# Optimization experiments

Measured on AMD Instinct MI355X. Metric: run time of the kernel, lower is better.

The kernel has to match this reference:

```python
import jax, jax.numpy as jnp
import numpy as np

B, S, D, H = 8, 1024, 512, 8
HD = D // H
NEG = -1000000000.0
LN_EPS = 1e-5


def setup_inputs() -> dict:
    key = jax.random.key(0)
    ks = jax.random.split(key, 16)
    sc = 0.02
    inp = {
        "query": jax.random.normal(ks[0], (B, S, D), jnp.float32),
        "inputs": jax.random.normal(ks[1], (B, S, D), jnp.float32),
        "ren_mat": jax.random.uniform(ks[2], (B, S, S), jnp.float32) * 5.0,
        "timestamp": jax.random.normal(ks[3], (B, S, S), jnp.float32),
        # causal mask: True where attention is disallowed (strictly upper triangular)
        "mask": jnp.triu(jnp.ones((1, S, S), jnp.bool_), k=1),
        "Wq": jax.random.normal(ks[4], (D, D), jnp.float32) * sc,
        "bq": jnp.zeros((D,), jnp.float32),
        "Wk": jax.random.normal(ks[5], (D, D), jnp.float32) * sc,
        "bk": jnp.zeros((D,), jnp.float32),
        "Wv": jax.random.normal(ks[6], (D, D), jnp.float32) * sc,
        "bv": jnp.zeros((D,), jnp.float32),
        "Wo": jax.random.normal(ks[7], (D, D), jnp.float32) * sc,
        "bo": jnp.zeros((D,), jnp.float32),
        "W1": jax.random.normal(ks[8], (D, D), jnp.float32) * sc,
        "b1": jnp.zeros((D,), jnp.float32),
        "ln_g": jnp.ones((D,), jnp.float32),
        "ln_b": jnp.zeros((D,), jnp.float32),
        "l1": jax.random.uniform(ks[9], (1,), jnp.float32),
    }
    return inp


def reference(query, inputs, ren_mat, timestamp, mask,
              Wq, bq, Wk, bk, Wv, bv, Wo, bo, W1, b1, ln_g, ln_b, l1):
    # QKV projections (qk_same=False path; q,k,v all computed from `inputs`)
    def proj(x, W, b):
        return (x @ W.T + b).reshape(B, S, H, HD).transpose(0, 2, 1, 3)  # (B,H,S,HD)

    q = proj(inputs, Wq, bq)
    k = proj(inputs, Wk, bk)
    v = proj(inputs, Wv, bv)

    m = mask[:, None]  # (1,1,S,S), broadcasts over batch & heads

    scores = jnp.einsum("bhqd,bhkd->bhqk", q, k) / jnp.sqrt(jnp.float32(HD))
    scores = jnp.where(m, NEG, scores)
    prob_attn = jax.nn.softmax(scores, axis=-1)

    # memory blend: log10(ren+1) and exp(-|t|), each masked, summed, softmaxed
    ren_feat = jnp.where(m, NEG, jnp.log10(ren_mat + 1.0)[:, None])      # (B,H,S,S)
    time_stamp = jnp.where(m, NEG, jnp.exp(-jnp.abs(timestamp))[:, None])
    mem_attn = jax.nn.softmax(ren_feat + time_stamp, axis=-1)

    l = l1  # (1,) learned blend coefficient
    prob_attn = (1.0 - l) * prob_attn + l * mem_attn

    out = jnp.einsum("bhqk,bhkd->bhqd", prob_attn, v)
    out = out.transpose(0, 2, 1, 3).reshape(B, S, D)
    out = out @ Wo.T + bo

    # residual FFN + layernorm (dropout disabled / eval mode)
    out = out + (out @ W1.T + b1)
    mu = jnp.mean(out, axis=-1, keepdims=True)
    var = jnp.var(out, axis=-1, keepdims=True)
    out = (out - mu) / jnp.sqrt(var + LN_EPS) * ln_g + ln_b
    return out
```

## Files before the change

kernel.cpp:

```cpp
#include <hip/hip_runtime.h>
#include <math.h>

constexpr int kB = 8, kS = 1024, kD = 512, kH = 8, kHD = 64;
constexpr int kM = kB * kS;

typedef __attribute__((ext_vector_type(8))) short s8v;
typedef __attribute__((ext_vector_type(4))) float f4v;
typedef __attribute__((ext_vector_type(4))) unsigned short u4v;

__device__ __forceinline__ unsigned short f2bf(float f) {
    union { float f; unsigned int u; } c; c.f = f;
    unsigned int u = c.u + 0x7FFFu + ((c.u >> 16) & 1u);
    return (unsigned short)(u >> 16);
}

__device__ __forceinline__ void gl2lds(const unsigned short* g, unsigned short* l) {
    __builtin_amdgcn_global_load_lds(
        (const __attribute__((address_space(1))) unsigned int*)g,
        (__attribute__((address_space(3))) unsigned int*)l, 16, 0, 0);
}

__global__ __launch_bounds__(256) void prep_kernel(
    const float* __restrict__ X, const float* __restrict__ Wq,
    const float* __restrict__ Wk, const float* __restrict__ Wv,
    const float* __restrict__ Wo, const float* __restrict__ W1,
    const float* __restrict__ ren, const float* __restrict__ ts,
    const float* __restrict__ bo_g,
    unsigned short* __restrict__ Xbf, unsigned short* __restrict__ Wqkv,
    unsigned short* __restrict__ WoT, unsigned short* __restrict__ W1bf,
    unsigned short* __restrict__ mem)
{
    __shared__ float red[4];
    const int t = threadIdx.x;
    if (blockIdx.x < 5120) {
        const int idx = blockIdx.x * 256 + t;
        const float* src; unsigned short* dst; int off; bool isw1 = false;
        if (idx < 1048576)      { src = X;  dst = Xbf;           off = idx; }
        else if (idx < 1114112) { src = Wq; dst = Wqkv;          off = idx - 1048576; }
        else if (idx < 1179648) { src = Wk; dst = Wqkv + 262144; off = idx - 1114112; }
        else if (idx < 1245184) { src = Wv; dst = Wqkv + 524288; off = idx - 1179648; }
        else                    { src = W1; dst = W1bf;          off = idx - 1245184; isw1 = true; }
        float4 v = ((const float4*)src)[off];
        if (isw1) {
            const int e0 = off * 4;
            const int row = e0 >> 9, col0 = e0 & 511;
            if (row >= col0 && row < col0 + 4) ((float*)&v)[row - col0] += 1.0f;
        }
        u4v p;
        p[0] = f2bf(v.x); p[1] = f2bf(v.y); p[2] = f2bf(v.z); p[3] = f2bf(v.w);
        ((u4v*)dst)[off] = p;
        return;
    }
    if (blockIdx.x >= 13312) {
        const int bi2 = blockIdx.x - 13312;
        if (bi2 < 64) {
            __shared__ float T[64][65];
            const int tr = bi2 >> 3, tc = bi2 & 7;
            const int rr0 = t >> 4, cc0 = (t & 15) * 4;
#pragma unroll
            for (int i2 = 0; i2 < 4; ++i2) {
                const int r = i2 * 16 + rr0;
                const float4 v = *(const float4*)&Wo[(size_t)(tr * 64 + r) * 512 + tc * 64 + cc0];
                T[r][cc0] = v.x; T[r][cc0 + 1] = v.y; T[r][cc0 + 2] = v.z; T[r][cc0 + 3] = v.w;
            }
            __syncthreads();
#pragma unroll
            for (int i2 = 0; i2 < 4; ++i2) {
                const int r2 = i2 * 16 + rr0;
                u4v p;
                p[0] = f2bf(T[cc0][r2]);     p[1] = f2bf(T[cc0 + 1][r2]);
                p[2] = f2bf(T[cc0 + 2][r2]); p[3] = f2bf(T[cc0 + 3][r2]);
                *(u4v*)&WoT[(size_t)(tc * 64 + r2) * 512 + tr * 64 + cc0] = p;
            }
        } else {
            WoT[262144 + t]       = f2bf(bo_g[t]);
            WoT[262144 + 256 + t] = f2bf(bo_g[t + 256]);
        }
        return;
    }
    const int bi = blockIdx.x - 5120;
    const int i = bi & (kS - 1);
    const float* renr = ren + (size_t)bi * kS;
    const float* tsr  = ts  + (size_t)bi * kS;
    unsigned short* memr = mem + (size_t)bi * kS;
    const int j0 = t * 4;
    const float4 r4 = *(const float4*)(renr + j0);
    const float4 t4 = *(const float4*)(tsr + j0);
    float rv[4] = {r4.x, r4.y, r4.z, r4.w};
    float tv[4] = {t4.x, t4.y, t4.z, t4.w};
    float p4[4];
    float lsum = 0.0f;
#pragma unroll
    for (int e = 0; e < 4; ++e) {
        const int j = j0 + e;
        float p = 0.0f;
        if (j <= i) {
            const float val = 0.30102999566f * __log2f(rv[e] + 1.0f) + __expf(-fabsf(tv[e]));
            p = __expf(val);
        }
        p4[e] = p;
        lsum += p;
    }
#pragma unroll
    for (int d = 1; d < 64; d <<= 1) lsum += __shfl_xor(lsum, d);
    if ((t & 63) == 0) red[t >> 6] = lsum;
    __syncthreads();
    const float Z = red[0] + red[1] + red[2] + red[3];
    const float inv = 1.0f / Z;
    u4v pk;
#pragma unroll
    for (int e = 0; e < 4; ++e) pk[e] = f2bf(p4[e] * inv);
    *(u4v*)(memr + j0) = pk;
}

template <int NT>
__device__ __forceinline__ void mfma_core2(
    const unsigned short* __restrict__ A, const unsigned short* __restrict__ B,
    int M0, int N0, unsigned short* As, unsigned short* Bs, f4v (&acc)[4][NT])
{
    const int t = threadIdx.x, w = t >> 6, lane = t & 63;
    const int l16 = lane & 15, quad = lane >> 4;
    const int wm = (w & 1) * 64, wn = (w >> 1) * (NT * 16);
    constexpr int NB = NT / 2;
    constexpr int ABUF = 128 * 32;
    constexpr int BBUF = NT * 32 * 32;

    const unsigned short* gA[2]; unsigned short* lA[2];
#pragma unroll
    for (int i = 0; i < 2; ++i) {
        const int r0 = w * 32 + i * 16;
        const int r = r0 + (lane >> 2);
        const int c = (lane & 3) ^ ((r >> 1) & 3);
        gA[i] = A + (size_t)(M0 + r) * 512 + c * 8;
        lA[i] = As + r0 * 32;
    }
    const unsigned short* gB[NB]; unsigned short* lB[NB];
#pragma unroll
    for (int i = 0; i < NB; ++i) {
        const int r0 = w * (16 * NB) + i * 16;
        const int r = r0 + (lane >> 2);
        const int c = (lane & 3) ^ ((r >> 1) & 3);
        gB[i] = B + (size_t)(N0 + r) * 512 + c * 8;
        lB[i] = Bs + r0 * 32;
    }

    const f4v zero = {0.0f, 0.0f, 0.0f, 0.0f};
#pragma unroll
    for (int mt = 0; mt < 4; ++mt)
#pragma unroll
        for (int nt = 0; nt < NT; ++nt) acc[mt][nt] = zero;

    gl2lds(gA[0], lA[0]);
    gl2lds(gA[1], lA[1]);
#pragma unroll
    for (int i = 0; i < NB; ++i) gl2lds(gB[i], lB[i]);

#pragma unroll 1
    for (int k0 = 0; k0 < 512; k0 += 32) {
        const int cur = (k0 >> 5) & 1;
        __syncthreads();
        if (k0 + 32 < 512) {
            const int nb = cur ^ 1;
            gl2lds(gA[0] + k0 + 32, lA[0] + nb * ABUF);
            gl2lds(gA[1] + k0 + 32, lA[1] + nb * ABUF);
#pragma unroll
            for (int i = 0; i < NB; ++i) gl2lds(gB[i] + k0 + 32, lB[i] + nb * BBUF);
        }
        s8v af[4], bf_[NT];
#pragma unroll
        for (int mt = 0; mt < 4; ++mt) {
            const int r = wm + mt * 16 + l16;
            const int p = r * 4 + (quad ^ ((r >> 1) & 3));
            af[mt] = *(const s8v*)&As[cur * ABUF + p * 8];
        }
#pragma unroll
        for (int nt = 0; nt < NT; ++nt) {
            const int r = wn + nt * 16 + l16;
            const int p = r * 4 + (quad ^ ((r >> 1) & 3));
            bf_[nt] = *(const s8v*)&Bs[cur * BBUF + p * 8];
        }
#pragma unroll
        for (int mt = 0; mt < 4; ++mt)
#pragma unroll
            for (int nt = 0; nt < NT; ++nt)
                acc[mt][nt] = __builtin_amdgcn_mfma_f32_16x16x32_bf16(
                    af[mt], bf_[nt], acc[mt][nt], 0, 0, 0);
    }
}

__global__ __launch_bounds__(256) void qkv_mfma_kernel(
    const unsigned short* __restrict__ Xbf, const unsigned short* __restrict__ Wqkv,
    const float* __restrict__ bq, const float* __restrict__ bk, const float* __restrict__ bv,
    const unsigned short* __restrict__ W1bf, const unsigned short* __restrict__ WoT,
    const float* __restrict__ b1,
    unsigned short* __restrict__ qbf, unsigned short* __restrict__ kbf,
    unsigned short* __restrict__ vTbf,
    unsigned short* __restrict__ Wcomb, float* __restrict__ bcomb)
{
    __shared__ __align__(16) unsigned short As[2 * 128 * 32];
    __shared__ __align__(16) unsigned short Bs[2 * 128 * 32];
    const int y = blockIdx.y;
    const int t = threadIdx.x, w = t >> 6, lane = t & 63;
    const int l16 = lane & 15, quad = lane >> 4;

    if (y == 12) {
        if (blockIdx.x >= 36) return;
        f4v acc[4][2];
        const int M0 = (blockIdx.x / 9) * 128, N0 = (blockIdx.x % 9) * 64;
        mfma_core2<2>(W1bf, WoT, M0, N0, As, Bs, acc);
        const int wm = (w & 1) * 64, wn = (w >> 1) * 32;
#pragma unroll
        for (int nt = 0; nt < 2; ++nt) {
            const int qq = N0 + wn + nt * 16 + l16;
#pragma unroll
            for (int mt = 0; mt < 4; ++mt)
#pragma unroll
                for (int rr = 0; rr < 4; ++rr) {
                    const int m = M0 + wm + mt * 16 + quad * 4 + rr;
                    if (qq < 512)       Wcomb[(size_t)m * 512 + qq] = f2bf(acc[mt][nt][rr]);
                    else if (qq == 512) bcomb[m] = acc[mt][nt][rr] + b1[m];
                }
        }
        return;
    }

    f4v acc[4][4];
    const int wm = (w & 1) * 64, wn = (w >> 1) * 64;
    if (y < 8) {
        const int M0 = blockIdx.x * 128, N0 = y * 128;
        mfma_core2<4>(Xbf, Wqkv, M0, N0, As, Bs, acc);
        const int z = N0 >> 9;
        const float* bias = (z == 0) ? bq : bk;
        unsigned short* out = (z == 0) ? qbf : kbf;
#pragma unroll
        for (int nt = 0; nt < 4; ++nt) {
            const int n512 = (N0 + wn + nt * 16 + l16) & 511;
            const int h = n512 >> 6, hd = n512 & 63;
            const float bv_ = bias[n512];
#pragma unroll
            for (int mt = 0; mt < 4; ++mt) {
#pragma unroll
                for (int rr = 0; rr < 4; ++rr) {
                    const int m = M0 + wm + mt * 16 + quad * 4 + rr;
                    const int b = m >> 10, s = m & (kS - 1);
                    out[(((size_t)b * kH + h) * kS + s) * kHD + hd] =
                        f2bf(acc[mt][nt][rr] + bv_);
                }
            }
        }
    } else {
        const int M0 = (y - 8) * 128, N0 = blockIdx.x * 128;
        mfma_core2<4>(Wqkv + (size_t)1024 * 512, Xbf, M0, N0, As, Bs, acc);
#pragma unroll
        for (int mt = 0; mt < 4; ++mt) {
#pragma unroll
            for (int rr = 0; rr < 4; ++rr) {
                const int vcol = M0 + wm + mt * 16 + quad * 4 + rr;
                const int h = vcol >> 6, hd = vcol & 63;
                const float bv_ = bv[vcol];
#pragma unroll
                for (int nt = 0; nt < 4; ++nt) {
                    const int sg = N0 + wn + nt * 16 + l16;
                    const int b = sg >> 10, s = sg & (kS - 1);
                    vTbf[(((size_t)b * kH + h) * kHD + hd) * kS + s] =
                        f2bf(acc[mt][nt][rr] + bv_);
                }
            }
        }
    }
}

__global__ __launch_bounds__(256) void gemm_final_kernel(
    const unsigned short* __restrict__ Abf, const unsigned short* __restrict__ Wcomb,
    const float* __restrict__ bcomb, float* __restrict__ out)
{
    __shared__ __align__(16) unsigned short As[2 * 128 * 32];
    __shared__ __align__(16) unsigned short Bs[2 * 64 * 32];
    f4v acc[4][2];
    const int M0 = blockIdx.x * 128, N0 = blockIdx.y * 64;
    mfma_core2<2>(Abf, Wcomb, M0, N0, As, Bs, acc);
    const int t = threadIdx.x, w = t >> 6, lane = t & 63;
    const int l16 = lane & 15, quad = lane >> 4;
    const int wm = (w & 1) * 64, wn = (w >> 1) * 32;
#pragma unroll
    for (int nt = 0; nt < 2; ++nt) {
        const int n = N0 + wn + nt * 16 + l16;
        const float bv_ = bcomb[n];
#pragma unroll
        for (int mt = 0; mt < 4; ++mt)
#pragma unroll
            for (int rr = 0; rr < 4; ++rr) {
                const int m = M0 + wm + mt * 16 + quad * 4 + rr;
                out[(size_t)m * kD + n] = acc[mt][nt][rr] + bv_;
            }
    }
}

#define KFRAG(tile, r, c) (*(const s8v*)&(tile)[(size_t)(r) * 64 + ((((c) ^ ((r) & 7))) << 3)])
#define VFRAG(tile, r, c) (*(const s8v*)&(tile)[(size_t)(r) * 128 + ((((c) ^ ((r) & 15))) << 3)])

__global__ __launch_bounds__(256, 2) void flash_attn_kernel(
    const unsigned short* __restrict__ q, const unsigned short* __restrict__ k,
    const unsigned short* __restrict__ vT, const unsigned short* __restrict__ mem,
    const float* __restrict__ l1, unsigned short* __restrict__ aout)
{
    const int bh = blockIdx.x;
    const int qt = 15 - blockIdx.y;
    const int b = bh >> 3, h = bh & 7;
    const int t = threadIdx.x;
    const int w = t >> 6, lane = t & 63;
    const int quad = lane >> 4, l16 = lane & 15;
    const float lam = l1[0];

    __shared__ __align__(16) unsigned short KV[2][2][64 * 128];
    __shared__ __align__(16) unsigned short P_lds[4][16 * 128];

    const int qbase = qt * 64;
    const unsigned short* qrow = q + ((size_t)bh * kS + qbase + w * 16 + l16) * kHD;
    const s8v qa0 = *(const s8v*)(qrow + quad * 8);
    const s8v qa1 = *(const s8v*)(qrow + 32 + quad * 8);
    const unsigned short* mbase = mem + ((size_t)b * kS + qbase + w * 16 + l16) * kS;

    const unsigned short* kb = k + (size_t)bh * kS * kHD;
    const unsigned short* vb = vT + (size_t)bh * kHD * kS;

    const int nkt = (qt >> 1) + 1;

    const unsigned short* gsrc[8];
    int gstep[8];
    unsigned short* ldst[8];
#pragma unroll
    for (int u = 0; u < 8; ++u) {
        const int seg = w * 8 + u;
        if (seg < 16) {
            const int s = seg;
            const int rloc = s * 8 + (lane >> 3);
            const int chunk = (lane & 7) ^ ((lane >> 3) & 7);
            gsrc[u] = kb + (size_t)rloc * kHD + chunk * 8;
            gstep[u] = 128 * kHD;
            ldst[u] = &KV[0][0][s * 512];
        } else {
            const int s = seg - 16;
            const int d = s * 4 + (lane >> 4);
            const int chunk = (lane & 15) ^ ((lane >> 4) & 3) ^ ((s & 3) << 2);
            gsrc[u] = vb + (size_t)d * kS + chunk * 8;
            gstep[u] = 128;
            ldst[u] = &KV[0][1][s * 512];
        }
    }

#pragma unroll
    for (int u = 0; u < 8; ++u) gl2lds(gsrc[u], ldst[u]);

    const f4v zero = {0.0f, 0.0f, 0.0f, 0.0f};
    f4v Oa[4], Om[4];
    float lr[4];
#pragma unroll
    for (int nt = 0; nt < 4; ++nt) { Oa[nt] = zero; Om[nt] = zero; lr[nt] = 0.0f; }

    for (int kt = 0; kt < nkt; ++kt) {
        __syncthreads();
        const int cur = kt & 1;
        if (kt + 1 < nkt) {
            const int boff = ((kt + 1) & 1) * 16384;
#pragma unroll
            for (int u = 0; u < 8; ++u)
                gl2lds(gsrc[u] + (size_t)(kt + 1) * gstep[u], ldst[u] + boff);
        }
        s8v ma[4];
#pragma unroll
        for (int ks = 0; ks < 4; ++ks)
            ma[ks] = *(const s8v*)(mbase + kt * 128 + ks * 32 + quad * 8);

        const unsigned short* Kc = &KV[cur][0][0];
        const unsigned short* Vc = &KV[cur][1][0];
        const bool last = (kt == nkt - 1);

#pragma unroll
        for (int ct = 0; ct < 8; ++ct) {
            const int r = ct * 16 + l16;
            const s8v kb0 = KFRAG(Kc, r, quad);
            const s8v kb1 = KFRAG(Kc, r, 4 + quad);
            f4v acc = zero;
            acc = __builtin_amdgcn_mfma_f32_16x16x32_bf16(qa0, kb0, acc, 0, 0, 0);
            acc = __builtin_amdgcn_mfma_f32_16x16x32_bf16(qa1, kb1, acc, 0, 0, 0);
#pragma unroll
            for (int rr = 0; rr < 4; ++rr) {
                float p = __expf(acc[rr] * 0.125f);
                if (last && (kt * 128 + r) > (qbase + w * 16 + quad * 4 + rr)) p = 0.0f;
                lr[rr] += p;
                const int pr = quad * 4 + rr;
                const int ck = ct * 2 + (l16 >> 3);
                P_lds[w][pr * 128 + (((ck ^ pr) & 15) << 3) + (l16 & 7)] = f2bf(p);
            }
        }
        s8v pa[4];
#pragma unroll
        for (int ks = 0; ks < 4; ++ks)
            pa[ks] = *(const s8v*)&P_lds[w][l16 * 128 + ((((ks * 4 + quad) ^ l16) & 15) << 3)];
#pragma unroll
        for (int nt = 0; nt < 4; ++nt) {
#pragma unroll
            for (int ks = 0; ks < 4; ++ks) {
                const s8v vfk = VFRAG(Vc, nt * 16 + l16, ks * 4 + quad);
                Oa[nt] = __builtin_amdgcn_mfma_f32_16x16x32_bf16(pa[ks], vfk, Oa[nt], 0, 0, 0);
                Om[nt] = __builtin_amdgcn_mfma_f32_16x16x32_bf16(ma[ks], vfk, Om[nt], 0, 0, 0);
            }
        }
    }

    float inv4[4];
#pragma unroll
    for (int rr = 0; rr < 4; ++rr) {
        float Z = lr[rr];
        Z += __shfl_xor(Z, 1);
        Z += __shfl_xor(Z, 2);
        Z += __shfl_xor(Z, 4);
        Z += __shfl_xor(Z, 8);
        inv4[rr] = (1.0f - lam) / Z;
    }
    const int r0 = qbase + w * 16;
#pragma unroll
    for (int nt = 0; nt < 4; ++nt)
#pragma unroll
        for (int rr = 0; rr < 4; ++rr) {
            const int i = r0 + quad * 4 + rr;
            const int d = h * kHD + nt * 16 + l16;
            aout[((size_t)b * kS + i) * kD + d] =
                f2bf(Oa[nt][rr] * inv4[rr] + lam * Om[nt][rr]);
        }
}

__global__ __launch_bounds__(256) void ln_kernel(
    const float* __restrict__ x, const float* __restrict__ g,
    const float* __restrict__ bb, float* __restrict__ out)
{
    const int row = blockIdx.x;
    const int t = threadIdx.x;
    const float* xr = x + (size_t)row * kD;
    float a = xr[t], c = xr[t + 256];
    __shared__ float red[256];
    float s1 = a + c, s2 = a * a + c * c;
    red[t] = s1;
    __syncthreads();
    for (int s = 128; s > 0; s >>= 1) {
        if (t < s) red[t] += red[t + s];
        __syncthreads();
    }
    const float sum = red[0];
    __syncthreads();
    red[t] = s2;
    __syncthreads();
    for (int s = 128; s > 0; s >>= 1) {
        if (t < s) red[t] += red[t + s];
        __syncthreads();
    }
    const float sq = red[0];
    float mu = sum * (1.0f / kD);
    float var = sq * (1.0f / kD) - mu * mu;
    float inv = rsqrtf(var + 1e-5f);
    out[(size_t)row * kD + t]       = (a - mu) * inv * g[t] + bb[t];
    out[(size_t)row * kD + t + 256] = (c - mu) * inv * g[t + 256] + bb[t + 256];
}

extern "C" void kernel_launch(void* const* d_in, const int* in_sizes, int n_in,
                              void* d_out, int out_size, void* d_ws, size_t ws_size,
                              hipStream_t stream) {
    const float* X   = (const float*)d_in[1];
    const float* ren = (const float*)d_in[2];
    const float* ts  = (const float*)d_in[3];
    const float* Wq = (const float*)d_in[5];  const float* bq = (const float*)d_in[6];
    const float* Wk = (const float*)d_in[7];  const float* bk = (const float*)d_in[8];
    const float* Wv = (const float*)d_in[9];  const float* bv = (const float*)d_in[10];
    const float* Wo = (const float*)d_in[11]; const float* bo = (const float*)d_in[12];
    const float* W1 = (const float*)d_in[13]; const float* b1 = (const float*)d_in[14];
    const float* lng = (const float*)d_in[15]; const float* lnb = (const float*)d_in[16];
    const float* l1 = (const float*)d_in[17];
    float* out = (float*)d_out;

    char* wsb = (char*)d_ws;
    unsigned short* Xbf    = (unsigned short*)(wsb);
    unsigned short* Wqkvbf = (unsigned short*)(wsb + (8u  << 20));
    unsigned short* WoTbf  = (unsigned short*)(wsb + (10u << 20));
    unsigned short* W1bf   = (unsigned short*)(wsb + (11u << 20));
    unsigned short* qbf    = (unsigned short*)(wsb + (12u << 20));
    unsigned short* kbf    = (unsigned short*)(wsb + (20u << 20));
    unsigned short* vTbf   = (unsigned short*)(wsb + (28u << 20));
    unsigned short* membf  = (unsigned short*)(wsb + (36u << 20));
    unsigned short* aoutbf = (unsigned short*)(wsb + (52u << 20));
    unsigned short* Wcombf = (unsigned short*)(wsb + (60u << 20));
    float*          bcombf = (float*)        (wsb + (61u << 20));

    prep_kernel<<<dim3(13377), 256, 0, stream>>>(
        X, Wq, Wk, Wv, Wo, W1, ren, ts, bo, Xbf, Wqkvbf, WoTbf, W1bf, membf);
    qkv_mfma_kernel<<<dim3(kM / 128, 13), 256, 0, stream>>>(
        Xbf, Wqkvbf, bq, bk, bv, W1bf, WoTbf, b1, qbf, kbf, vTbf, Wcombf, bcombf);
    flash_attn_kernel<<<dim3(64, 16), 256, 0, stream>>>(
        qbf, kbf, vTbf, membf, l1, aoutbf);
    gemm_final_kernel<<<dim3(kM / 128, kD / 64), 256, 0, stream>>>(
        aoutbf, Wcombf, bcombf, out);
    ln_kernel<<<dim3(kM), 256, 0, stream>>>(out, lng, lnb, out);
}
```

Baseline: 249.1 us.

## Fuse final GEMM with layernorm, pair causal query tiles, skip masked mem loads

Replaces the separate output GEMM and layernorm kernels with one kernel where each block computes a full 32x512 row tile and reduces mean and variance in registers and shared memory. This removes the fp32 round trip of the pre-norm output. The attention kernel now pairs a high and a low causal query tile in each block so every block does the same amount of work and the K/V tiles are loaded once for both. The prep kernel also skips reading ren and timestamp for fully masked column chunks. In exchange, the fused GEMM launches fewer, larger blocks, and the attention kernel holds two sets of accumulators, which raises register pressure.

```diff
diff --git a/kernel.cpp b/kernel.cpp
--- a/kernel.cpp
+++ b/kernel.cpp
@@ -84,22 +84,24 @@
     const float* tsr  = ts  + (size_t)bi * kS;
     unsigned short* memr = mem + (size_t)bi * kS;
     const int j0 = t * 4;
-    const float4 r4 = *(const float4*)(renr + j0);
-    const float4 t4 = *(const float4*)(tsr + j0);
-    float rv[4] = {r4.x, r4.y, r4.z, r4.w};
-    float tv[4] = {t4.x, t4.y, t4.z, t4.w};
-    float p4[4];
+    float p4[4] = {0.0f, 0.0f, 0.0f, 0.0f};
     float lsum = 0.0f;
-#pragma unroll
-    for (int e = 0; e < 4; ++e) {
-        const int j = j0 + e;
-        float p = 0.0f;
-        if (j <= i) {
-            const float val = 0.30102999566f * __log2f(rv[e] + 1.0f) + __expf(-fabsf(tv[e]));
-            p = __expf(val);
-        }
-        p4[e] = p;
-        lsum += p;
+    if (j0 <= i) {
+        const float4 r4 = *(const float4*)(renr + j0);
+        const float4 t4 = *(const float4*)(tsr + j0);
+        float rv[4] = {r4.x, r4.y, r4.z, r4.w};
+        float tv[4] = {t4.x, t4.y, t4.z, t4.w};
+#pragma unroll
+        for (int e = 0; e < 4; ++e) {
+            const int j = j0 + e;
+            float p = 0.0f;
+            if (j <= i) {
+                const float val = 0.30102999566f * __log2f(rv[e] + 1.0f) + __expf(-fabsf(tv[e]));
+                p = __expf(val);
+            }
+            p4[e] = p;
+            lsum += p;
+        }
     }
 #pragma unroll
     for (int d = 1; d < 64; d <<= 1) lsum += __shfl_xor(lsum, d);
@@ -270,30 +272,135 @@
     }
 }
 
-__global__ __launch_bounds__(256) void gemm_final_kernel(
+__global__ __launch_bounds__(512, 2) void gemm_ln_kernel(
     const unsigned short* __restrict__ Abf, const unsigned short* __restrict__ Wcomb,
-    const float* __restrict__ bcomb, float* __restrict__ out)
+    const float* __restrict__ bcomb, const float* __restrict__ g,
+    const float* __restrict__ bb, float* __restrict__ out)
 {
-    __shared__ __align__(16) unsigned short As[2 * 128 * 32];
-    __shared__ __align__(16) unsigned short Bs[2 * 64 * 32];
-    f4v acc[4][2];
-    const int M0 = blockIdx.x * 128, N0 = blockIdx.y * 64;
-    mfma_core2<2>(Abf, Wcomb, M0, N0, As, Bs, acc);
+    __shared__ __align__(16) unsigned short As[2 * 32 * 32];
+    __shared__ __align__(16) unsigned short Bs[2 * 512 * 32];
+    constexpr int ABUF = 32 * 32, BBUF = 512 * 32;
     const int t = threadIdx.x, w = t >> 6, lane = t & 63;
     const int l16 = lane & 15, quad = lane >> 4;
-    const int wm = (w & 1) * 64, wn = (w >> 1) * 32;
-#pragma unroll
-    for (int nt = 0; nt < 2; ++nt) {
-        const int n = N0 + wn + nt * 16 + l16;
-        const float bv_ = bcomb[n];
-#pragma unroll
-        for (int mt = 0; mt < 4; ++mt)
-#pragma unroll
-            for (int rr = 0; rr < 4; ++rr) {
-                const int m = M0 + wm + mt * 16 + quad * 4 + rr;
-                out[(size_t)m * kD + n] = acc[mt][nt][rr] + bv_;
-            }
-    }
+    const int M0 = blockIdx.x * 32;
+
+    const unsigned short* gB[4]; unsigned short* lB[4];
+#pragma unroll
+    for (int i = 0; i < 4; ++i) {
+        const int r0 = w * 64 + i * 16;
+        const int r = r0 + (lane >> 2);
+        const int c = (lane & 3) ^ ((r >> 1) & 3);
+        gB[i] = Wcomb + (size_t)r * 512 + c * 8;
+        lB[i] = Bs + r0 * 32;
+    }
+    const unsigned short* gA = nullptr; unsigned short* lA = nullptr;
+    if (w < 2) {
+        const int r0 = w * 16;
+        const int r = r0 + (lane >> 2);
+        const int c = (lane & 3) ^ ((r >> 1) & 3);
+        gA = Abf + (size_t)(M0 + r) * 512 + c * 8;
+        lA = As + r0 * 32;
+    }
+
+    const f4v zero = {0.0f, 0.0f, 0.0f, 0.0f};
+    f4v acc[2][4];
+#pragma unroll
+    for (int mt = 0; mt < 2; ++mt)
+#pragma unroll
+        for (int nt = 0; nt < 4; ++nt) acc[mt][nt] = zero;
+
+#pragma unroll
+    for (int i = 0; i < 4; ++i) gl2lds(gB[i], lB[i]);
+    if (w < 2) gl2lds(gA, lA);
+
+#pragma unroll 1
+    for (int k0 = 0; k0 < 512; k0 += 32) {
+        const int cur = (k0 >> 5) & 1;
+        __syncthreads();
+        if (k0 + 32 < 512) {
+            const int nb = cur ^ 1;
+#pragma unroll
+            for (int i = 0; i < 4; ++i) gl2lds(gB[i] + k0 + 32, lB[i] + nb * BBUF);
+            if (w < 2) gl2lds(gA + k0 + 32, lA + nb * ABUF);
+        }
+        s8v af[2], bf_[4];
+#pragma unroll
+        for (int mt = 0; mt < 2; ++mt) {
+            const int r = mt * 16 + l16;
+            const int p = r * 4 + (quad ^ ((r >> 1) & 3));
+            af[mt] = *(const s8v*)&As[cur * ABUF + p * 8];
+        }
+#pragma unroll
+        for (int nt = 0; nt < 4; ++nt) {
+            const int r = w * 64 + nt * 16 + l16;
+            const int p = r * 4 + (quad ^ ((r >> 1) & 3));
+            bf_[nt] = *(const s8v*)&Bs[cur * BBUF + p * 8];
+        }
+#pragma unroll
+        for (int mt = 0; mt < 2; ++mt)
+#pragma unroll
+            for (int nt = 0; nt < 4; ++nt)
+                acc[mt][nt] = __builtin_amdgcn_mfma_f32_16x16x32_bf16(
+                    af[mt], bf_[nt], acc[mt][nt], 0, 0, 0);
+    }
+
+    float bias[4], gg[4], bbv[4];
+#pragma unroll
+    for (int nt = 0; nt < 4; ++nt) {
+        const int n = w * 64 + nt * 16 + l16;
+        bias[nt] = bcomb[n]; gg[nt] = g[n]; bbv[nt] = bb[n];
+    }
+#pragma unroll
+    for (int mt = 0; mt < 2; ++mt)
+#pragma unroll
+        for (int nt = 0; nt < 4; ++nt)
+#pragma unroll
+            for (int rr = 0; rr < 4; ++rr) acc[mt][nt][rr] += bias[nt];
+
+    float2* red = (float2*)Bs;
+    float2* stats = (float2*)As;
+#pragma unroll
+    for (int mt = 0; mt < 2; ++mt)
+#pragma unroll
+        for (int rr = 0; rr < 4; ++rr) {
+            float s = 0.0f, qq = 0.0f;
+#pragma unroll
+            for (int nt = 0; nt < 4; ++nt) {
+                const float v = acc[mt][nt][rr];
+                s += v; qq += v * v;
+            }
+            s += __shfl_xor(s, 1); qq += __shfl_xor(qq, 1);
+            s += __shfl_xor(s, 2); qq += __shfl_xor(qq, 2);
+            s += __shfl_xor(s, 4); qq += __shfl_xor(qq, 4);
+            s += __shfl_xor(s, 8); qq += __shfl_xor(qq, 8);
+            if (l16 == 0) red[w * 32 + mt * 16 + quad * 4 + rr] = make_float2(s, qq);
+        }
+    __syncthreads();
+    if (t < 32) {
+        float s = 0.0f, qq = 0.0f;
+#pragma unroll
+        for (int wv = 0; wv < 8; ++wv) {
+            const float2 f2 = red[wv * 32 + t];
+            s += f2.x; qq += f2.y;
+        }
+        const float mu = s * (1.0f / kD);
+        const float var = qq * (1.0f / kD) - mu * mu;
+        stats[t] = make_float2(mu, rsqrtf(var + 1e-5f));
+    }
+    __syncthreads();
+#pragma unroll
+    for (int mt = 0; mt < 2; ++mt)
+#pragma unroll
+        for (int rr = 0; rr < 4; ++rr) {
+            const int row = mt * 16 + quad * 4 + rr;
+            const float2 st = stats[row];
+#pragma unroll
+            for (int nt = 0; nt < 4; ++nt) {
+                const int n = w * 64 + nt * 16 + l16;
+                out[(size_t)(M0 + row) * kD + n] =
+                    (acc[mt][nt][rr] - st.x) * st.y * gg[nt] + bbv[nt];
+            }
+        }
 }
 
 #define KFRAG(tile, r, c) (*(const s8v*)&(tile)[(size_t)(r) * 64 + ((((c) ^ ((r) & 7))) << 3)])
@@ -304,9 +411,10 @@
     const unsigned short* __restrict__ vT, const unsigned short* __restrict__ mem,
     const float* __restrict__ l1, unsigned short* __restrict__ aout)
 {
-    const int bh = blockIdx.x;
-    const int qt = 15 - blockIdx.y;
-    const int b = bh >> 3, h = bh & 7;
+    const int qp = blockIdx.x;
+    const int hi = 15 - qp, lo = qp;
+    const int h = blockIdx.y, b = blockIdx.z;
+    const int bh = b * kH + h;
     const int t = threadIdx.x;
     const int w = t >> 6, lane = t & 63;
     const int quad = lane >> 4, l16 = lane & 15;
@@ -315,16 +423,22 @@
     __shared__ __align__(16) unsigned short KV[2][2][64 * 128];
     __shared__ __align__(16) unsigned short P_lds[4][16 * 128];
 
-    const int qbase = qt * 64;
-    const unsigned short* qrow = q + ((size_t)bh * kS + qbase + w * 16 + l16) * kHD;
-    const s8v qa0 = *(const s8v*)(qrow + quad * 8);
-    const s8v qa1 = *(const s8v*)(qrow + 32 + quad * 8);
-    const unsigned short* mbase = mem + ((size_t)b * kS + qbase + w * 16 + l16) * kS;
+    const int tbase[2] = {hi * 64, lo * 64};
+    s8v qa[2][2];
+    const unsigned short* mbase[2];
+#pragma unroll
+    for (int ti = 0; ti < 2; ++ti) {
+        const unsigned short* qrow = q + ((size_t)bh * kS + tbase[ti] + w * 16 + l16) * kHD;
+        qa[ti][0] = *(const s8v*)(qrow + quad * 8);
+        qa[ti][1] = *(const s8v*)(qrow + 32 + quad * 8);
+        mbase[ti] = mem + ((size_t)b * kS + tbase[ti] + w * 16 + l16) * kS;
+    }
 
     const unsigned short* kb = k + (size_t)bh * kS * kHD;
     const unsigned short* vb = vT + (size_t)bh * kHD * kS;
 
-    const int nkt = (qt >> 1) + 1;
+    const int nkt   = (hi >> 1) + 1;
+    const int nktlo = (lo >> 1) + 1;
 
     const unsigned short* gsrc[8];
     int gstep[8];
@@ -353,10 +467,14 @@
     for (int u = 0; u < 8; ++u) gl2lds(gsrc[u], ldst[u]);
 
     const f4v zero = {0.0f, 0.0f, 0.0f, 0.0f};
-    f4v Oa[4], Om[4];
-    float lr[4];
-#pragma unroll
-    for (int nt = 0; nt < 4; ++nt) { Oa[nt] = zero; Om[nt] = zero; lr[nt] = 0.0f; }
+    f4v Oa[2][4], Om[2][4];
+    float lr[2][4];
+#pragma unroll
+    for (int ti = 0; ti < 2; ++ti)
+#pragma unroll
+        for (int nt = 0; nt < 4; ++nt) {
+            Oa[ti][nt] = zero; Om[ti][nt] = zero; lr[ti][nt] = 0.0f;
+        }
 
     for (int kt = 0; kt < nkt; ++kt) {
         __syncthreads();
@@ -367,100 +485,107 @@
             for (int u = 0; u < 8; ++u)
                 gl2lds(gsrc[u] + (size_t)(kt + 1) * gstep[u], ldst[u] + boff);
         }
-        s8v ma[4];
+        const bool alo = (kt < nktlo);
+        s8v ma0[4], ma1[4];
 #pragma unroll
         for (int ks = 0; ks < 4; ++ks)
-            ma[ks] = *(const s8v*)(mbase + kt * 128 + ks * 32 + quad * 8);
-
+            ma0[ks] = *(const s8v*)(mbase[0] + kt * 128 + ks * 32 + quad * 8);
+        if (alo) {
+#pragma unroll
+            for (int ks = 0; ks < 4; ++ks)
+                ma1[ks] = *(const s8v*)(mbase[1] + kt * 128 + ks * 32 + quad * 8);
+        }
         const unsigned short* Kc = &KV[cur][0][0];
         const unsigned short* Vc = &KV[cur][1][0];
-        const bool last = (kt == nkt - 1);
-
-#pragma unroll
-        for (int ct = 0; ct < 8; ++ct) {
-            const int r = ct * 16 + l16;
-            const s8v kb0 = KFRAG(Kc, r, quad);
-            const s8v kb1 = KFRAG(Kc, r, 4 + quad);
-            f4v acc = zero;
-            acc = __builtin_amdgcn_mfma_f32_16x16x32_bf16(qa0, kb0, acc, 0, 0, 0);
-            acc = __builtin_amdgcn_mfma_f32_16x16x32_bf16(qa1, kb1, acc, 0, 0, 0);
-#pragma unroll
-            for (int rr = 0; rr < 4; ++rr) {
-                float p = __expf(acc[rr] * 0.125f);
-                if (last && (kt * 128 + r) > (qbase + w * 16 + quad * 4 + rr)) p = 0.0f;
-                lr[rr] += p;
-                const int pr = quad * 4 + rr;
-                const int ck = ct * 2 + (l16 >> 3);
-                P_lds[w][pr * 128 + (((ck ^ pr) & 15) << 3) + (l16 & 7)] = f2bf(p);
-            }
-        }
-        s8v pa[4];
-#pragma unroll
-        for (int ks = 0; ks < 4; ++ks)
-            pa[ks] = *(const s8v*)&P_lds[w][l16 * 128 + ((((ks * 4 + quad) ^ l16) & 15) << 3)];
+
+        s8v pa0[4], pa1[4];
+        {
+            const bool diag = (kt == nkt - 1);
+#pragma unroll
+            for (int ct = 0; ct < 8; ++ct) {
+                const int r = ct * 16 + l16;
+                const s8v kb0 = KFRAG(Kc, r, quad);
+                const s8v kb1 = KFRAG(Kc, r, 4 + quad);
+                f4v acc = zero;
+                acc = __builtin_amdgcn_mfma_f32_16x16x32_bf16(qa[0][0], kb0, acc, 0, 0, 0);
+                acc = __builtin_amdgcn_mfma_f32_16x16x32_bf16(qa[0][1], kb1, acc, 0, 0, 0);
+#pragma unroll
+                for (int rr = 0; rr < 4; ++rr) {
+                    float p = __expf(acc[rr] * 0.125f);
+                    if (diag && (kt * 128 + r) > (tbase[0] + w * 16 + quad * 4 + rr)) p = 0.0f;
+                    lr[0][rr] += p;
+                    const int pr = quad * 4 + rr;
+                    const int ck = ct * 2 + (l16 >> 3);
+                    P_lds[w][pr * 128 + (((ck ^ pr) & 15) << 3) + (l16 & 7)] = f2bf(p);
+                }
+            }
+#pragma unroll
+            for (int ks = 0; ks < 4; ++ks)
+                pa0[ks] = *(const s8v*)&P_lds[w][l16 * 128 + ((((ks * 4 + quad) ^ l16) & 15) << 3)];
+        }
+        if (alo) {
+            const bool diag = (kt == nktlo - 1);
+#pragma unroll
+            for (int ct = 0; ct < 8; ++ct) {
+                const int r = ct * 16 + l16;
+                const s8v kb0 = KFRAG(Kc, r, quad);
+                const s8v kb1 = KFRAG(Kc, r, 4 + quad);
+                f4v acc = zero;
+                acc = __builtin_amdgcn_mfma_f32_16x16x32_bf16(qa[1][0], kb0, acc, 0, 0, 0);
+                acc = __builtin_amdgcn_mfma_f32_16x16x32_bf16(qa[1][1], kb1, acc, 0, 0, 0);
+#pragma unroll
+                for (int rr = 0; rr < 4; ++rr) {
+                    float p = __expf(acc[rr] * 0.125f);
+                    if (diag && (kt * 128 + r) > (tbase[1] + w * 16 + quad * 4 + rr)) p = 0.0f;
+                    lr[1][rr] += p;
+                    const int pr = quad * 4 + rr;
+                    const int ck = ct * 2 + (l16 >> 3);
+                    P_lds[w][pr * 128 + (((ck ^ pr) & 15) << 3) + (l16 & 7)] = f2bf(p);
+                }
+            }
+#pragma unroll
+            for (int ks = 0; ks < 4; ++ks)
+                pa1[ks] = *(const s8v*)&P_lds[w][l16 * 128 + ((((ks * 4 + quad) ^ l16) & 15) << 3)];
+        }
+
 #pragma unroll
         for (int nt = 0; nt < 4; ++nt) {
 #pragma unroll
             for (int ks = 0; ks < 4; ++ks) {
                 const s8v vfk = VFRAG(Vc, nt * 16 + l16, ks * 4 + quad);
-                Oa[nt] = __builtin_amdgcn_mfma_f32_16x16x32_bf16(pa[ks], vfk, Oa[nt], 0, 0, 0);
-                Om[nt] = __builtin_amdgcn_mfma_f32_16x16x32_bf16(ma[ks], vfk, Om[nt], 0, 0, 0);
-            }
-        }
-    }
-
-    float inv4[4];
-#pragma unroll
-    for (int rr = 0; rr < 4; ++rr) {
-        float Z = lr[rr];
-        Z += __shfl_xor(Z, 1);
-        Z += __shfl_xor(Z, 2);
-        Z += __shfl_xor(Z, 4);
-        Z += __shfl_xor(Z, 8);
-        inv4[rr] = (1.0f - lam) / Z;
-    }
-    const int r0 = qbase + w * 16;
-#pragma unroll
-    for (int nt = 0; nt < 4; ++nt)
+                Oa[0][nt] = __builtin_amdgcn_mfma_f32_16x16x32_bf16(pa0[ks], vfk, Oa[0][nt], 0, 0, 0);
+                Om[0][nt] = __builtin_amdgcn_mfma_f32_16x16x32_bf16(ma0[ks], vfk, Om[0][nt], 0, 0, 0);
+                if (alo) {
+                    Oa[1][nt] = __builtin_amdgcn_mfma_f32_16x16x32_bf16(pa1[ks], vfk, Oa[1][nt], 0, 0, 0);
+                    Om[1][nt] = __builtin_amdgcn_mfma_f32_16x16x32_bf16(ma1[ks], vfk, Om[1][nt], 0, 0, 0);
+                }
+            }
+        }
+    }
+
+#pragma unroll
+    for (int ti = 0; ti < 2; ++ti) {
+        float inv4[4];
 #pragma unroll
         for (int rr = 0; rr < 4; ++rr) {
-            const int i = r0 + quad * 4 + rr;
-            const int d = h * kHD + nt * 16 + l16;
-            aout[((size_t)b * kS + i) * kD + d] =
-                f2bf(Oa[nt][rr] * inv4[rr] + lam * Om[nt][rr]);
-        }
-}
-
-__global__ __launch_bounds__(256) void ln_kernel(
-    const float* __restrict__ x, const float* __restrict__ g,
-    const float* __restrict__ bb, float* __restrict__ out)
-{
-    const int row = blockIdx.x;
-    const int t = threadIdx.x;
-    const float* xr = x + (size_t)row * kD;
-    float a = xr[t], c = xr[t + 256];
-    __shared__ float red[256];
-    float s1 = a + c, s2 = a * a + c * c;
-    red[t] = s1;
-    __syncthreads();
-    for (int s = 128; s > 0; s >>= 1) {
-        if (t < s) red[t] += red[t + s];
-        __syncthreads();
-    }
-    const float sum = red[0];
-    __syncthreads();
-    red[t] = s2;
-    __syncthreads();
-    for (int s = 128; s > 0; s >>= 1) {
-        if (t < s) red[t] += red[t + s];
-        __syncthreads();
-    }
-    const float sq = red[0];
-    float mu = sum * (1.0f / kD);
-    float var = sq * (1.0f / kD) - mu * mu;
-    float inv = rsqrtf(var + 1e-5f);
-    out[(size_t)row * kD + t]       = (a - mu) * inv * g[t] + bb[t];
-    out[(size_t)row * kD + t + 256] = (c - mu) * inv * g[t + 256] + bb[t + 256];
+            float Z = lr[ti][rr];
+            Z += __shfl_xor(Z, 1);
+            Z += __shfl_xor(Z, 2);
+            Z += __shfl_xor(Z, 4);
+            Z += __shfl_xor(Z, 8);
+            inv4[rr] = (1.0f - lam) / Z;
+        }
+        const int r0 = tbase[ti] + w * 16;
+#pragma unroll
+        for (int nt = 0; nt < 4; ++nt)
+#pragma unroll
+            for (int rr = 0; rr < 4; ++rr) {
+                const int i = r0 + quad * 4 + rr;
+                const int d = h * kHD + nt * 16 + l16;
+                aout[((size_t)b * kS + i) * kD + d] =
+                    f2bf(Oa[ti][nt][rr] * inv4[rr] + lam * Om[ti][nt][rr]);
+            }
+    }
 }
 
 extern "C" void kernel_launch(void* const* d_in, const int* in_sizes, int n_in,
@@ -495,9 +620,8 @@
         X, Wq, Wk, Wv, Wo, W1, ren, ts, bo, Xbf, Wqkvbf, WoTbf, W1bf, membf);
     qkv_mfma_kernel<<<dim3(kM / 128, 13), 256, 0, stream>>>(
         Xbf, Wqkvbf, bq, bk, bv, W1bf, WoTbf, b1, qbf, kbf, vTbf, Wcombf, bcombf);
-    flash_attn_kernel<<<dim3(64, 16), 256, 0, stream>>>(
+    flash_attn_kernel<<<dim3(8, kH, kB), 256, 0, stream>>>(
         qbf, kbf, vTbf, membf, l1, aoutbf);
-    gemm_final_kernel<<<dim3(kM / 128, kD / 64), 256, 0, stream>>>(
-        aoutbf, Wcombf, bcombf, out);
-    ln_kernel<<<dim3(kM), 256, 0, stream>>>(out, lng, lnb, out);
-}
+    gemm_ln_kernel<<<dim3(kM / 32), 512, 0, stream>>>(
+        aoutbf, Wcombf, bcombf, lng, lnb, out);
+}
```

Result: slower. 287.7 us (+15.5%).
